# Optimization experiments

Measured on AMD Instinct MI355X. Metric: run time of the kernel, lower is better.

## Reference

```python
import jax, jax.numpy as jnp
import numpy as np

B, C, H, W = 4, 256, 64, 64
CQK = C // 8  # qk_downscale = 8


def setup_inputs() -> dict:
    key = jax.random.key(0)
    ks = jax.random.split(key, 4)
    scale = 0.02
    x = jax.random.normal(ks[0], (B, C, H, W), dtype=jnp.float32)
    Wq = jax.random.normal(ks[1], (CQK, C), dtype=jnp.float32) * scale
    bq = jnp.zeros((CQK,), dtype=jnp.float32)
    Wk = jax.random.normal(ks[2], (CQK, C), dtype=jnp.float32) * scale
    bk = jnp.zeros((CQK,), dtype=jnp.float32)
    Wv = jax.random.normal(ks[3], (C, C), dtype=jnp.float32) * scale
    bv = jnp.zeros((C,), dtype=jnp.float32)
    gamma = jnp.ones((1,), dtype=jnp.float32)
    return {"x": x, "Wq": Wq, "bq": bq, "Wk": Wk, "bk": bk,
            "Wv": Wv, "bv": bv, "gamma": gamma}


def reference(x, Wq, bq, Wk, bk, Wv, bv, gamma):
    b, c, h, w = x.shape
    n = h * w
    xf = x.reshape(b, c, n)                                   # [B,C,N]
    # 1x1 Conv1d == per-position linear projection
    q = jnp.einsum('oc,bcn->bon', Wq, xf) + bq[:, None]        # [B,C/8,N]
    k = jnp.einsum('oc,bcn->bon', Wk, xf) + bk[:, None]        # [B,C/8,N]
    v = jnp.einsum('oc,bcn->bon', Wv, xf) + bv[:, None]        # [B,C,N]
    # scores[b,i,j] = sum_c q[b,c,i] * k[b,c,j]  (bmm(q^T, k))
    scores = jnp.einsum('bci,bcj->bij', q, k)                  # [B,N,N]
    # softmax over dim=1 (the i / contracted axis) — SAGAN style, no 1/sqrt(d)
    attn = jax.nn.softmax(scores, axis=1)                      # [B,N,N]
    out = gamma * jnp.einsum('bcn,bnm->bcm', v, attn) + xf     # [B,C,N]
    return out.reshape(b, c, h, w)
```

## Files before the change

### kernel.cpp

```cpp
#include <hip/hip_runtime.h>
#include <stdint.h>

typedef __attribute__((ext_vector_type(8))) short short8;
typedef __attribute__((ext_vector_type(4))) float f32x4;
typedef __attribute__((ext_vector_type(4))) unsigned int u32x4;

#define MFMA16(a, b, c) __builtin_amdgcn_mfma_f32_16x16x32_bf16((a), (b), (c), 0, 0, 0)

#define GLOAD_LDS16(gsrc, ldst)                                                        \
    __builtin_amdgcn_global_load_lds(                                                  \
        (const __attribute__((address_space(1))) unsigned int*)(gsrc),                 \
        (__attribute__((address_space(3))) unsigned int*)(ldst), 16, 0, 0)

#define LOG2E 1.4426950408889634f

static __device__ __forceinline__ unsigned short f2bf(float f) {
    union { float f; unsigned int u; } v; v.f = f;
    unsigned int u = v.u;
    unsigned int r = 0x7fffu + ((u >> 16) & 1u);
    return (unsigned short)((u + r) >> 16);
}

static __device__ __forceinline__ float bf2f(unsigned short s) {
    union { unsigned int u; float f; } v; v.u = ((unsigned int)s) << 16;
    return v.f;
}

static __device__ __forceinline__ unsigned int cvt_pk_bf16(float lo, float hi) {
    unsigned int r;
    asm("v_cvt_pk_bf16_f32 %0, %1, %2" : "=v"(r) : "v"(lo), "v"(hi));
    return r;
}

static __device__ __forceinline__ float fexp2(float x) {
#if __has_builtin(__builtin_amdgcn_exp2f)
    return __builtin_amdgcn_exp2f(x);
#else
    return exp2f(x);
#endif
}

__global__ __launch_bounds__(256) void k_prepw(const float* __restrict__ Wq,
                                               const float* __restrict__ Wk,
                                               const float* __restrict__ Wv,
                                               unsigned short* __restrict__ Wb) {
    const int i = (blockIdx.x * 256 + threadIdx.x) * 4;
    const float* src; int off;
    if (i < 8192)       { src = Wq; off = i; }
    else if (i < 16384) { src = Wk; off = i - 8192; }
    else                { src = Wv; off = i - 16384; }
    const float4 v = *(const float4*)(src + off);
    ushort4 o;
    o.x = f2bf(v.x); o.y = f2bf(v.y); o.z = f2bf(v.z); o.w = f2bf(v.w);
    *(ushort4*)(Wb + i) = o;
}

__global__ __launch_bounds__(256) void k_qkv(const float* __restrict__ x,
                                             const unsigned short* __restrict__ Wb,
                                             const float* __restrict__ bq,
                                             const float* __restrict__ bk,
                                             const float* __restrict__ bv,
                                             unsigned short* __restrict__ qT,
                                             unsigned short* __restrict__ kT,
                                             unsigned short* __restrict__ vp) {
    const int b = blockIdx.y;
    const int nt = blockIdx.x;
    const int h = blockIdx.z;
    const int lane = threadIdx.x & 63;
    const int wv = threadIdx.x >> 6;
    const int l15 = lane & 15, g = lane >> 4;
    const int n0 = nt * 64;
    const int nw = n0 + wv * 16;

    const float* xb = x + (size_t)b * 1048576;
    const float* xs = xb + (size_t)(g * 8) * 4096 + nw + l15;

    const unsigned short* Wqb = Wb;
    const unsigned short* Wkb = Wb + 8192;
    const unsigned short* Wvb = Wb + 16384 + h * 32768;

    f32x4 aqk[4] = {};
    f32x4 av[8] = {};

#pragma unroll 2
    for (int k0 = 0; k0 < 256; k0 += 32) {
        const float* xp = xs + (size_t)k0 * 4096;
        float xv[8];
#pragma unroll
        for (int j = 0; j < 8; ++j) xv[j] = xp[(size_t)j * 4096];
        const u32x4 ux = {cvt_pk_bf16(xv[0], xv[1]), cvt_pk_bf16(xv[2], xv[3]),
                          cvt_pk_bf16(xv[4], xv[5]), cvt_pk_bf16(xv[6], xv[7])};
        const short8 xa = __builtin_bit_cast(short8, ux);

        if (h == 0) {
#pragma unroll
            for (int ot = 0; ot < 4; ++ot) {
                const unsigned short* wr = (ot < 2) ? (Wqb + (size_t)(ot * 16 + l15) * 256)
                                                    : (Wkb + (size_t)((ot - 2) * 16 + l15) * 256);
                const short8 wb8 = *(const short8*)(wr + k0 + g * 8);
                aqk[ot] = MFMA16(xa, wb8, aqk[ot]);
            }
        }
#pragma unroll
        for (int ct = 0; ct < 8; ++ct) {
            const short8 wv8 = *(const short8*)(Wvb + (size_t)(ct * 16 + l15) * 256 + k0 + g * 8);
            av[ct] = MFMA16(wv8, xa, av[ct]);
        }
    }

    if (h == 0) {
#pragma unroll
        for (int ot = 0; ot < 4; ++ot) {
            const int o = (ot & 1) * 16 + l15;
            const float bias = (ot < 2) ? bq[o] : bk[o];
            const float sc = (ot < 2) ? LOG2E : 1.0f;
            unsigned short* dst = (ot < 2) ? qT : kT;
#pragma unroll
            for (int r = 0; r < 4; ++r) {
                const int n = nw + g * 4 + r;
                dst[((size_t)b * 4096 + n) * 32 + o] = f2bf((aqk[ot][r] + bias) * sc);
            }
        }
    }
    const int jp = ((wv >> 1) * 4 + (l15 >> 2)) * 8 + (wv & 1) * 4 + (l15 & 3);
#pragma unroll
    for (int ct = 0; ct < 8; ++ct)
#pragma unroll
        for (int r = 0; r < 4; ++r) {
            const int c = h * 128 + ct * 16 + g * 4 + r;
            vp[((size_t)b * 256 + c) * 4096 + n0 + jp] = f2bf(av[ct][r] + bv[c]);
        }
}

__global__ __launch_bounds__(256, 2) void k_attn(const unsigned short* __restrict__ qT,
                                                 const unsigned short* __restrict__ kT,
                                                 const unsigned short* __restrict__ vp,
                                                 unsigned short* __restrict__ Opart,
                                                 float* __restrict__ mll,
                                                 int ilen) {
    __shared__ __align__(16) unsigned short vlds[2 * 16384];

    const int b = blockIdx.y;
    const int mt = blockIdx.x;
    const int sp = blockIdx.z;
    const int tid = threadIdx.x;
    const int lane = tid & 63;
    const int wv = tid >> 6;
    const int l15 = lane & 15, g = lane >> 4;
    const int m_base = mt * 128 + wv * 32;
    const int i_start = sp * ilen;
    const int T = ilen >> 6;

    const unsigned short* qTb = qT + (size_t)b * 131072;
    const unsigned short* vpb = vp + (size_t)b * 1048576;

    const short8 qkB0 = *(const short8*)(kT + ((size_t)b * 4096 + m_base + l15) * 32 + g * 8);
    const short8 qkB1 = *(const short8*)(kT + ((size_t)b * 4096 + m_base + 16 + l15) * 32 + g * 8);

    const int jd = (lane & 7) ^ ((lane >> 3) & 7);
    const unsigned short* vsrc = vpb + (size_t)(64 * wv + (lane >> 3)) * 4096 + i_start + jd * 8;
    const int ldst0 = wv * 4096;

#define STAGE(bufsel, ioff)                                                             \
    do {                                                                                \
        _Pragma("unroll")                                                               \
        for (int s_ = 0; s_ < 8; ++s_)                                                  \
            GLOAD_LDS16(vsrc + (size_t)s_ * 32768 + (ioff),                             \
                        vlds + (bufsel) * 16384 + ldst0 + s_ * 512);                    \
    } while (0)

    const int rdA = l15 * 64 + ((g ^ (l15 & 7)) << 3);
    const int rdB = l15 * 64 + (((4 + g) ^ (l15 & 7)) << 3);

    const unsigned short* qp = qTb + (size_t)(i_start + l15) * 32 + g * 8;

    f32x4 oacc[16][2] = {};
    float l_acc0 = 0.0f, l_acc1 = 0.0f;
    const f32x4 zf = {0.f, 0.f, 0.f, 0.f};

    STAGE(0, 0);
    __syncthreads();

    for (int t = 0; t < T; ++t) {
        const int cur = t & 1;
        if (t + 1 < T) STAGE(cur ^ 1, (t + 1) * 64);

        const short8 a0 = *(const short8*)(qp);
        const short8 a1 = *(const short8*)(qp + 512);
        const short8 a2 = *(const short8*)(qp + 1024);
        const short8 a3 = *(const short8*)(qp + 1536);
        qp += 2048;
        f32x4 P[4][2];
        P[0][0] = MFMA16(a0, qkB0, zf); P[0][1] = MFMA16(a0, qkB1, zf);
        P[1][0] = MFMA16(a1, qkB0, zf); P[1][1] = MFMA16(a1, qkB1, zf);
        P[2][0] = MFMA16(a2, qkB0, zf); P[2][1] = MFMA16(a2, qkB1, zf);
        P[3][0] = MFMA16(a3, qkB0, zf); P[3][1] = MFMA16(a3, qkB1, zf);

        float s00 = 0.f, s01 = 0.f, s10 = 0.f, s11 = 0.f;
#pragma unroll
        for (int it = 0; it < 4; ++it)
#pragma unroll
            for (int r = 0; r < 4; ++r) {
                P[it][0][r] = fexp2(P[it][0][r]);
                P[it][1][r] = fexp2(P[it][1][r]);
                if (it < 2) { s00 += P[it][0][r]; s01 += P[it][1][r]; }
                else        { s10 += P[it][0][r]; s11 += P[it][1][r]; }
            }
        l_acc0 += s00 + s10;
        l_acc1 += s01 + s11;

        const u32x4 u00 = {cvt_pk_bf16(P[0][0][0], P[0][0][1]), cvt_pk_bf16(P[0][0][2], P[0][0][3]),
                           cvt_pk_bf16(P[1][0][0], P[1][0][1]), cvt_pk_bf16(P[1][0][2], P[1][0][3])};
        const u32x4 u01 = {cvt_pk_bf16(P[0][1][0], P[0][1][1]), cvt_pk_bf16(P[0][1][2], P[0][1][3]),
                           cvt_pk_bf16(P[1][1][0], P[1][1][1]), cvt_pk_bf16(P[1][1][2], P[1][1][3])};
        const u32x4 u10 = {cvt_pk_bf16(P[2][0][0], P[2][0][1]), cvt_pk_bf16(P[2][0][2], P[2][0][3]),
                           cvt_pk_bf16(P[3][0][0], P[3][0][1]), cvt_pk_bf16(P[3][0][2], P[3][0][3])};
        const u32x4 u11 = {cvt_pk_bf16(P[2][1][0], P[2][1][1]), cvt_pk_bf16(P[2][1][2], P[2][1][3]),
                           cvt_pk_bf16(P[3][1][0], P[3][1][1]), cvt_pk_bf16(P[3][1][2], P[3][1][3])};
        const short8 pb00 = __builtin_bit_cast(short8, u00);
        const short8 pb01 = __builtin_bit_cast(short8, u01);
        const short8 pb10 = __builtin_bit_cast(short8, u10);
        const short8 pb11 = __builtin_bit_cast(short8, u11);

        const unsigned short* vbase = vlds + cur * 16384;
        const unsigned short* pA = vbase + rdA;
        const unsigned short* pB = vbase + rdB;
        __builtin_amdgcn_s_setprio(1);
#pragma unroll
        for (int ct = 0; ct < 16; ++ct) {
            const short8 va0 = *(const short8*)(pA + ct * 1024);
            const short8 va1 = *(const short8*)(pB + ct * 1024);
            oacc[ct][0] = MFMA16(va0, pb00, oacc[ct][0]);
            oacc[ct][1] = MFMA16(va0, pb01, oacc[ct][1]);
            oacc[ct][0] = MFMA16(va1, pb10, oacc[ct][0]);
            oacc[ct][1] = MFMA16(va1, pb11, oacc[ct][1]);
        }
        __builtin_amdgcn_s_setprio(0);

        if (t + 1 < T) __syncthreads();
    }
#undef STAGE

    unsigned short* Ob = Opart + (size_t)(sp * 4 + b) * 1048576;
#pragma unroll
    for (int ct = 0; ct < 16; ++ct)
#pragma unroll
        for (int r = 0; r < 4; ++r) {
            const int c = ct * 16 + g * 4 + r;
            Ob[(size_t)c * 4096 + m_base + l15]      = f2bf(oacc[ct][0][r]);
            Ob[(size_t)c * 4096 + m_base + 16 + l15] = f2bf(oacc[ct][1][r]);
        }
    float l0 = l_acc0, l1 = l_acc1;
    l0 += __shfl_xor(l0, 16); l0 += __shfl_xor(l0, 32);
    l1 += __shfl_xor(l1, 16); l1 += __shfl_xor(l1, 32);
    if (lane < 16) {
        const size_t mi = (size_t)(sp * 4 + b) * 4096 + m_base + l15;
        mll[mi]      = l0;
        mll[mi + 16] = l1;
    }
}

__global__ __launch_bounds__(256) void k_combine(const unsigned short* __restrict__ Opart,
                                                 const float* __restrict__ mll,
                                                 const float* __restrict__ x,
                                                 const float* __restrict__ gamma,
                                                 float* __restrict__ out, int S) {
    const size_t e0 = ((size_t)blockIdx.x * 256 + threadIdx.x) * 8;
    const int m0 = (int)(e0 & 4095);
    const int b = (int)(e0 >> 20);

    float L[8] = {}, O[8] = {};
    for (int s = 0; s < S; ++s) {
        const size_t base = (size_t)(s * 4 + b) * 4096 + m0;
        const float4 la = *(const float4*)(mll + base);
        const float4 lc = *(const float4*)(mll + base + 4);
        const short8 op = *(const short8*)(Opart + (size_t)s * 4194304 + e0);
        L[0] += la.x; O[0] += bf2f((unsigned short)op[0]);
        L[1] += la.y; O[1] += bf2f((unsigned short)op[1]);
        L[2] += la.z; O[2] += bf2f((unsigned short)op[2]);
        L[3] += la.w; O[3] += bf2f((unsigned short)op[3]);
        L[4] += lc.x; O[4] += bf2f((unsigned short)op[4]);
        L[5] += lc.y; O[5] += bf2f((unsigned short)op[5]);
        L[6] += lc.z; O[6] += bf2f((unsigned short)op[6]);
        L[7] += lc.w; O[7] += bf2f((unsigned short)op[7]);
    }

    const float g0 = gamma[0];
    const float4 x0 = *(const float4*)(x + e0);
    const float4 x1 = *(const float4*)(x + e0 + 4);
    float4 o0, o1;
    o0.x = g0 * O[0] / L[0] + x0.x; o0.y = g0 * O[1] / L[1] + x0.y;
    o0.z = g0 * O[2] / L[2] + x0.z; o0.w = g0 * O[3] / L[3] + x0.w;
    o1.x = g0 * O[4] / L[4] + x1.x; o1.y = g0 * O[5] / L[5] + x1.y;
    o1.z = g0 * O[6] / L[6] + x1.z; o1.w = g0 * O[7] / L[7] + x1.w;
    *(float4*)(out + e0) = o0;
    *(float4*)(out + e0 + 4) = o1;
}

extern "C" void kernel_launch(void* const* d_in, const int* in_sizes, int n_in,
                              void* d_out, int out_size, void* d_ws, size_t ws_size,
                              hipStream_t stream) {
    (void)in_sizes; (void)n_in; (void)out_size;
    const float* x     = (const float*)d_in[0];
    const float* Wq    = (const float*)d_in[1];
    const float* bq    = (const float*)d_in[2];
    const float* Wk    = (const float*)d_in[3];
    const float* bk    = (const float*)d_in[4];
    const float* Wv    = (const float*)d_in[5];
    const float* bv    = (const float*)d_in[6];
    const float* gamma = (const float*)d_in[7];
    float* out = (float*)d_out;

    unsigned short* qT = (unsigned short*)d_ws;
    unsigned short* kT = qT + (size_t)4 * 4096 * 32;
    unsigned short* vp = kT + (size_t)4 * 4096 * 32;
    unsigned short* Wb = vp + (size_t)4 * 256 * 4096;
    unsigned short* Opart = Wb + 81920;

    const size_t base_el = 2 * (size_t)4 * 4096 * 32 + (size_t)4 * 256 * 4096 + 81920;
    auto need = [&](int s) {
        return (base_el + (size_t)s * 4194304) * 2 + (size_t)s * 16384 * 4;
    };
    const int S = (need(4) <= ws_size) ? 4 : (need(2) <= ws_size) ? 2 : 1;
    float* mll = (float*)(Opart + (size_t)S * 4194304);

    k_prepw<<<dim3(80), 256, 0, stream>>>(Wq, Wk, Wv, Wb);
    k_qkv<<<dim3(64, 4, 2), 256, 0, stream>>>(x, Wb, bq, bk, bv, qT, kT, vp);
    k_attn<<<dim3(32, 4, S), 256, 0, stream>>>(qT, kT, vp, Opart, mll, 4096 / S);
    k_combine<<<dim3(2048), 256, 0, stream>>>(Opart, mll, x, gamma, out, S);
}
```

Before: 84.35 us.

## Switch attention kernel to 32x32x16 MFMA tiles with matching V permutation

Rewrites the attention inner loop to use 32x32x16 bf16 MFMA instead of 16x16x32, so each wave computes one 32-column score tile and accumulates output in 8 f32x16 accumulators. The V projection output permutation and the LDS read offsets are changed to match the new operand layout, and the row-sum reduction shrinks to a single shuffle. The aim is fewer MFMA issues and fewer LDS reads per unit of work, and higher operand reuse. The cost is a different register pressure profile and a dependent chain of four MFMAs per accumulator.

New measurement: 86.41 us. 2.4% more time.

```diff
diff --git a/kernel.cpp b/kernel.cpp
--- a/kernel.cpp
+++ b/kernel.cpp
@@ -3,9 +3,11 @@
 
 typedef __attribute__((ext_vector_type(8))) short short8;
 typedef __attribute__((ext_vector_type(4))) float f32x4;
+typedef __attribute__((ext_vector_type(16))) float f32x16;
 typedef __attribute__((ext_vector_type(4))) unsigned int u32x4;
 
 #define MFMA16(a, b, c) __builtin_amdgcn_mfma_f32_16x16x32_bf16((a), (b), (c), 0, 0, 0)
+#define MFMA32(a, b, c) __builtin_amdgcn_mfma_f32_32x32x16_bf16((a), (b), (c), 0, 0, 0)
 
 #define GLOAD_LDS16(gsrc, ldst)                                                        \
     __builtin_amdgcn_global_load_lds(                                                  \
@@ -122,7 +124,7 @@
             }
         }
     }
-    const int jp = ((wv >> 1) * 4 + (l15 >> 2)) * 8 + (wv & 1) * 4 + (l15 & 3);
+    const int jp = (2 * wv + ((l15 >> 2) & 1)) * 8 + (l15 & 3) + ((l15 >> 3) << 2);
 #pragma unroll
     for (int ct = 0; ct < 8; ++ct)
 #pragma unroll
@@ -146,7 +148,7 @@
     const int tid = threadIdx.x;
     const int lane = tid & 63;
     const int wv = tid >> 6;
-    const int l15 = lane & 15, g = lane >> 4;
+    const int l31 = lane & 31, h = lane >> 5;
     const int m_base = mt * 128 + wv * 32;
     const int i_start = sp * ilen;
     const int T = ilen >> 6;
@@ -154,8 +156,9 @@
     const unsigned short* qTb = qT + (size_t)b * 131072;
     const unsigned short* vpb = vp + (size_t)b * 1048576;
 
-    const short8 qkB0 = *(const short8*)(kT + ((size_t)b * 4096 + m_base + l15) * 32 + g * 8);
-    const short8 qkB1 = *(const short8*)(kT + ((size_t)b * 4096 + m_base + 16 + l15) * 32 + g * 8);
+    const unsigned short* krow = kT + ((size_t)b * 4096 + m_base + l31) * 32 + h * 8;
+    const short8 qkB0 = *(const short8*)(krow);
+    const short8 qkB1 = *(const short8*)(krow + 16);
 
     const int jd = (lane & 7) ^ ((lane >> 3) & 7);
     const unsigned short* vsrc = vpb + (size_t)(64 * wv + (lane >> 3)) * 4096 + i_start + jd * 8;
@@ -169,14 +172,18 @@
                         vlds + (bufsel) * 16384 + ldst0 + s_ * 512);                    \
     } while (0)
 
-    const int rdA = l15 * 64 + ((g ^ (l15 & 7)) << 3);
-    const int rdB = l15 * 64 + (((4 + g) ^ (l15 & 7)) << 3);
-
-    const unsigned short* qp = qTb + (size_t)(i_start + l15) * 32 + g * 8;
-
-    f32x4 oacc[16][2] = {};
-    float l_acc0 = 0.0f, l_acc1 = 0.0f;
-    const f32x4 zf = {0.f, 0.f, 0.f, 0.f};
+    const int rd0 = l31 * 64 + (((2 * 0 + h) ^ (l31 & 7)) << 3);
+    const int rd1 = l31 * 64 + (((2 * 1 + h) ^ (l31 & 7)) << 3);
+    const int rd2 = l31 * 64 + (((2 * 2 + h) ^ (l31 & 7)) << 3);
+    const int rd3 = l31 * 64 + (((2 * 3 + h) ^ (l31 & 7)) << 3);
+
+    const unsigned short* qp = qTb + (size_t)(i_start + l31) * 32 + h * 8;
+
+    f32x16 oacc[8] = {};
+    float l_acc = 0.0f;
+    f32x16 zf16;
+#pragma unroll
+    for (int r = 0; r < 16; ++r) zf16[r] = 0.0f;
 
     STAGE(0, 0);
     __syncthreads();
@@ -185,55 +192,50 @@
         const int cur = t & 1;
         if (t + 1 < T) STAGE(cur ^ 1, (t + 1) * 64);
 
-        const short8 a0 = *(const short8*)(qp);
-        const short8 a1 = *(const short8*)(qp + 512);
-        const short8 a2 = *(const short8*)(qp + 1024);
-        const short8 a3 = *(const short8*)(qp + 1536);
+        const short8 qa00 = *(const short8*)(qp);
+        const short8 qa01 = *(const short8*)(qp + 16);
+        const short8 qa10 = *(const short8*)(qp + 1024);
+        const short8 qa11 = *(const short8*)(qp + 1040);
         qp += 2048;
-        f32x4 P[4][2];
-        P[0][0] = MFMA16(a0, qkB0, zf); P[0][1] = MFMA16(a0, qkB1, zf);
-        P[1][0] = MFMA16(a1, qkB0, zf); P[1][1] = MFMA16(a1, qkB1, zf);
-        P[2][0] = MFMA16(a2, qkB0, zf); P[2][1] = MFMA16(a2, qkB1, zf);
-        P[3][0] = MFMA16(a3, qkB0, zf); P[3][1] = MFMA16(a3, qkB1, zf);
-
-        float s00 = 0.f, s01 = 0.f, s10 = 0.f, s11 = 0.f;
-#pragma unroll
-        for (int it = 0; it < 4; ++it)
-#pragma unroll
-            for (int r = 0; r < 4; ++r) {
-                P[it][0][r] = fexp2(P[it][0][r]);
-                P[it][1][r] = fexp2(P[it][1][r]);
-                if (it < 2) { s00 += P[it][0][r]; s01 += P[it][1][r]; }
-                else        { s10 += P[it][0][r]; s11 += P[it][1][r]; }
-            }
-        l_acc0 += s00 + s10;
-        l_acc1 += s01 + s11;
-
-        const u32x4 u00 = {cvt_pk_bf16(P[0][0][0], P[0][0][1]), cvt_pk_bf16(P[0][0][2], P[0][0][3]),
-                           cvt_pk_bf16(P[1][0][0], P[1][0][1]), cvt_pk_bf16(P[1][0][2], P[1][0][3])};
-        const u32x4 u01 = {cvt_pk_bf16(P[0][1][0], P[0][1][1]), cvt_pk_bf16(P[0][1][2], P[0][1][3]),
-                           cvt_pk_bf16(P[1][1][0], P[1][1][1]), cvt_pk_bf16(P[1][1][2], P[1][1][3])};
-        const u32x4 u10 = {cvt_pk_bf16(P[2][0][0], P[2][0][1]), cvt_pk_bf16(P[2][0][2], P[2][0][3]),
-                           cvt_pk_bf16(P[3][0][0], P[3][0][1]), cvt_pk_bf16(P[3][0][2], P[3][0][3])};
-        const u32x4 u11 = {cvt_pk_bf16(P[2][1][0], P[2][1][1]), cvt_pk_bf16(P[2][1][2], P[2][1][3]),
-                           cvt_pk_bf16(P[3][1][0], P[3][1][1]), cvt_pk_bf16(P[3][1][2], P[3][1][3])};
-        const short8 pb00 = __builtin_bit_cast(short8, u00);
-        const short8 pb01 = __builtin_bit_cast(short8, u01);
-        const short8 pb10 = __builtin_bit_cast(short8, u10);
-        const short8 pb11 = __builtin_bit_cast(short8, u11);
-
-        const unsigned short* vbase = vlds + cur * 16384;
-        const unsigned short* pA = vbase + rdA;
-        const unsigned short* pB = vbase + rdB;
+        f32x16 P0 = MFMA32(qa00, qkB0, zf16);
+        P0 = MFMA32(qa01, qkB1, P0);
+        f32x16 P1 = MFMA32(qa10, qkB0, zf16);
+        P1 = MFMA32(qa11, qkB1, P1);
+
+        float s = 0.f;
+#pragma unroll
+        for (int r = 0; r < 16; ++r) {
+            P0[r] = fexp2(P0[r]); s += P0[r];
+            P1[r] = fexp2(P1[r]); s += P1[r];
+        }
+        l_acc += s;
+
+        const u32x4 u0 = {cvt_pk_bf16(P0[0], P0[1]), cvt_pk_bf16(P0[2], P0[3]),
+                          cvt_pk_bf16(P0[4], P0[5]), cvt_pk_bf16(P0[6], P0[7])};
+        const u32x4 u1 = {cvt_pk_bf16(P0[8], P0[9]), cvt_pk_bf16(P0[10], P0[11]),
+                          cvt_pk_bf16(P0[12], P0[13]), cvt_pk_bf16(P0[14], P0[15])};
+        const u32x4 u2 = {cvt_pk_bf16(P1[0], P1[1]), cvt_pk_bf16(P1[2], P1[3]),
+                          cvt_pk_bf16(P1[4], P1[5]), cvt_pk_bf16(P1[6], P1[7])};
+        const u32x4 u3 = {cvt_pk_bf16(P1[8], P1[9]), cvt_pk_bf16(P1[10], P1[11]),
+                          cvt_pk_bf16(P1[12], P1[13]), cvt_pk_bf16(P1[14], P1[15])};
+        const short8 pb0 = __builtin_bit_cast(short8, u0);
+        const short8 pb1 = __builtin_bit_cast(short8, u1);
+        const short8 pb2 = __builtin_bit_cast(short8, u2);
+        const short8 pb3 = __builtin_bit_cast(short8, u3);
+
+        const unsigned short* vb = vlds + cur * 16384;
         __builtin_amdgcn_s_setprio(1);
 #pragma unroll
-        for (int ct = 0; ct < 16; ++ct) {
-            const short8 va0 = *(const short8*)(pA + ct * 1024);
-            const short8 va1 = *(const short8*)(pB + ct * 1024);
-            oacc[ct][0] = MFMA16(va0, pb00, oacc[ct][0]);
-            oacc[ct][1] = MFMA16(va0, pb01, oacc[ct][1]);
-            oacc[ct][0] = MFMA16(va1, pb10, oacc[ct][0]);
-            oacc[ct][1] = MFMA16(va1, pb11, oacc[ct][1]);
+        for (int cb = 0; cb < 8; ++cb) {
+            const unsigned short* vr = vb + cb * 2048;
+            const short8 va0 = *(const short8*)(vr + rd0);
+            const short8 va1 = *(const short8*)(vr + rd1);
+            const short8 va2 = *(const short8*)(vr + rd2);
+            const short8 va3 = *(const short8*)(vr + rd3);
+            oacc[cb] = MFMA32(va0, pb0, oacc[cb]);
+            oacc[cb] = MFMA32(va1, pb1, oacc[cb]);
+            oacc[cb] = MFMA32(va2, pb2, oacc[cb]);
+            oacc[cb] = MFMA32(va3, pb3, oacc[cb]);
         }
         __builtin_amdgcn_s_setprio(0);
 
@@ -243,20 +245,15 @@
 
     unsigned short* Ob = Opart + (size_t)(sp * 4 + b) * 1048576;
 #pragma unroll
-    for (int ct = 0; ct < 16; ++ct)
-#pragma unroll
-        for (int r = 0; r < 4; ++r) {
-            const int c = ct * 16 + g * 4 + r;
-            Ob[(size_t)c * 4096 + m_base + l15]      = f2bf(oacc[ct][0][r]);
-            Ob[(size_t)c * 4096 + m_base + 16 + l15] = f2bf(oacc[ct][1][r]);
-        }
-    float l0 = l_acc0, l1 = l_acc1;
-    l0 += __shfl_xor(l0, 16); l0 += __shfl_xor(l0, 32);
-    l1 += __shfl_xor(l1, 16); l1 += __shfl_xor(l1, 32);
-    if (lane < 16) {
-        const size_t mi = (size_t)(sp * 4 + b) * 4096 + m_base + l15;
-        mll[mi]      = l0;
-        mll[mi + 16] = l1;
+    for (int cb = 0; cb < 8; ++cb)
+#pragma unroll
+        for (int r = 0; r < 16; ++r) {
+            const int c = cb * 32 + (r & 3) + 8 * (r >> 2) + 4 * h;
+            Ob[(size_t)c * 4096 + m_base + l31] = f2bf(oacc[cb][r]);
+        }
+    float l0 = l_acc + __shfl_xor(l_acc, 32);
+    if (lane < 32) {
+        mll[(size_t)(sp * 4 + b) * 4096 + m_base + l31] = l0;
     }
 }
 
```

## Split attention K-tile across wave pairs with LDS reduction of accumulators

Applied to the files above, without the earlier changes.

k_attn now launches 512 threads per block, and each pair of waves splits the 64-wide i-chunk of each tile in half. Each wave computes half the scores and exp values and does half the PV MFMAs, and each wave also stages half as much V into LDS. At the end the two halves' fp32 accumulators and row sums are added through LDS in two passes before one wave writes the result. The aim is more waves in flight per block to hide latency, at the cost of extra barriers, an LDS reduction epilogue, and only one block per CU under the launch bounds.

Result: slower. 105.8 us (+25.5%).

```diff
diff --git a/kernel.cpp b/kernel.cpp
--- a/kernel.cpp
+++ b/kernel.cpp
@@ -132,7 +132,7 @@
         }
 }
 
-__global__ __launch_bounds__(256, 2) void k_attn(const unsigned short* __restrict__ qT,
+__global__ __launch_bounds__(512, 1) void k_attn(const unsigned short* __restrict__ qT,
                                                  const unsigned short* __restrict__ kT,
                                                  const unsigned short* __restrict__ vp,
                                                  unsigned short* __restrict__ Opart,
@@ -146,8 +146,9 @@
     const int tid = threadIdx.x;
     const int lane = tid & 63;
     const int wv = tid >> 6;
+    const int mg = wv >> 1, sl = wv & 1;
     const int l15 = lane & 15, g = lane >> 4;
-    const int m_base = mt * 128 + wv * 32;
+    const int m_base = mt * 128 + mg * 32;
     const int i_start = sp * ilen;
     const int T = ilen >> 6;
 
@@ -158,21 +159,20 @@
     const short8 qkB1 = *(const short8*)(kT + ((size_t)b * 4096 + m_base + 16 + l15) * 32 + g * 8);
 
     const int jd = (lane & 7) ^ ((lane >> 3) & 7);
-    const unsigned short* vsrc = vpb + (size_t)(64 * wv + (lane >> 3)) * 4096 + i_start + jd * 8;
-    const int ldst0 = wv * 4096;
+    const unsigned short* vsrc = vpb + (size_t)(32 * wv + (lane >> 3)) * 4096 + i_start + jd * 8;
+    const int ldst0 = wv * 2048;
 
 #define STAGE(bufsel, ioff)                                                             \
     do {                                                                                \
         _Pragma("unroll")                                                               \
-        for (int s_ = 0; s_ < 8; ++s_)                                                  \
+        for (int s_ = 0; s_ < 4; ++s_)                                                  \
             GLOAD_LDS16(vsrc + (size_t)s_ * 32768 + (ioff),                             \
                         vlds + (bufsel) * 16384 + ldst0 + s_ * 512);                    \
     } while (0)
 
-    const int rdA = l15 * 64 + ((g ^ (l15 & 7)) << 3);
-    const int rdB = l15 * 64 + (((4 + g) ^ (l15 & 7)) << 3);
-
-    const unsigned short* qp = qTb + (size_t)(i_start + l15) * 32 + g * 8;
+    const int rdA = l15 * 64 + (((4 * sl + g) ^ (l15 & 7)) << 3);
+
+    const unsigned short* qp = qTb + (size_t)(i_start + sl * 32 + l15) * 32 + g * 8;
 
     f32x4 oacc[16][2] = {};
     float l_acc0 = 0.0f, l_acc1 = 0.0f;
@@ -187,53 +187,36 @@
 
         const short8 a0 = *(const short8*)(qp);
         const short8 a1 = *(const short8*)(qp + 512);
-        const short8 a2 = *(const short8*)(qp + 1024);
-        const short8 a3 = *(const short8*)(qp + 1536);
         qp += 2048;
-        f32x4 P[4][2];
+        f32x4 P[2][2];
         P[0][0] = MFMA16(a0, qkB0, zf); P[0][1] = MFMA16(a0, qkB1, zf);
         P[1][0] = MFMA16(a1, qkB0, zf); P[1][1] = MFMA16(a1, qkB1, zf);
-        P[2][0] = MFMA16(a2, qkB0, zf); P[2][1] = MFMA16(a2, qkB1, zf);
-        P[3][0] = MFMA16(a3, qkB0, zf); P[3][1] = MFMA16(a3, qkB1, zf);
-
-        float s00 = 0.f, s01 = 0.f, s10 = 0.f, s11 = 0.f;
-#pragma unroll
-        for (int it = 0; it < 4; ++it)
+
+        float s0 = 0.f, s1 = 0.f;
+#pragma unroll
+        for (int it = 0; it < 2; ++it)
 #pragma unroll
             for (int r = 0; r < 4; ++r) {
-                P[it][0][r] = fexp2(P[it][0][r]);
-                P[it][1][r] = fexp2(P[it][1][r]);
-                if (it < 2) { s00 += P[it][0][r]; s01 += P[it][1][r]; }
-                else        { s10 += P[it][0][r]; s11 += P[it][1][r]; }
-            }
-        l_acc0 += s00 + s10;
-        l_acc1 += s01 + s11;
-
-        const u32x4 u00 = {cvt_pk_bf16(P[0][0][0], P[0][0][1]), cvt_pk_bf16(P[0][0][2], P[0][0][3]),
-                           cvt_pk_bf16(P[1][0][0], P[1][0][1]), cvt_pk_bf16(P[1][0][2], P[1][0][3])};
-        const u32x4 u01 = {cvt_pk_bf16(P[0][1][0], P[0][1][1]), cvt_pk_bf16(P[0][1][2], P[0][1][3]),
-                           cvt_pk_bf16(P[1][1][0], P[1][1][1]), cvt_pk_bf16(P[1][1][2], P[1][1][3])};
-        const u32x4 u10 = {cvt_pk_bf16(P[2][0][0], P[2][0][1]), cvt_pk_bf16(P[2][0][2], P[2][0][3]),
-                           cvt_pk_bf16(P[3][0][0], P[3][0][1]), cvt_pk_bf16(P[3][0][2], P[3][0][3])};
-        const u32x4 u11 = {cvt_pk_bf16(P[2][1][0], P[2][1][1]), cvt_pk_bf16(P[2][1][2], P[2][1][3]),
-                           cvt_pk_bf16(P[3][1][0], P[3][1][1]), cvt_pk_bf16(P[3][1][2], P[3][1][3])};
-        const short8 pb00 = __builtin_bit_cast(short8, u00);
-        const short8 pb01 = __builtin_bit_cast(short8, u01);
-        const short8 pb10 = __builtin_bit_cast(short8, u10);
-        const short8 pb11 = __builtin_bit_cast(short8, u11);
-
-        const unsigned short* vbase = vlds + cur * 16384;
-        const unsigned short* pA = vbase + rdA;
-        const unsigned short* pB = vbase + rdB;
+                P[it][0][r] = fexp2(P[it][0][r]); s0 += P[it][0][r];
+                P[it][1][r] = fexp2(P[it][1][r]); s1 += P[it][1][r];
+            }
+        l_acc0 += s0;
+        l_acc1 += s1;
+
+        const u32x4 u0 = {cvt_pk_bf16(P[0][0][0], P[0][0][1]), cvt_pk_bf16(P[0][0][2], P[0][0][3]),
+                          cvt_pk_bf16(P[1][0][0], P[1][0][1]), cvt_pk_bf16(P[1][0][2], P[1][0][3])};
+        const u32x4 u1 = {cvt_pk_bf16(P[0][1][0], P[0][1][1]), cvt_pk_bf16(P[0][1][2], P[0][1][3]),
+                          cvt_pk_bf16(P[1][1][0], P[1][1][1]), cvt_pk_bf16(P[1][1][2], P[1][1][3])};
+        const short8 pb0 = __builtin_bit_cast(short8, u0);
+        const short8 pb1 = __builtin_bit_cast(short8, u1);
+
+        const unsigned short* pA = vlds + cur * 16384 + rdA;
         __builtin_amdgcn_s_setprio(1);
 #pragma unroll
         for (int ct = 0; ct < 16; ++ct) {
-            const short8 va0 = *(const short8*)(pA + ct * 1024);
-            const short8 va1 = *(const short8*)(pB + ct * 1024);
-            oacc[ct][0] = MFMA16(va0, pb00, oacc[ct][0]);
-            oacc[ct][1] = MFMA16(va0, pb01, oacc[ct][1]);
-            oacc[ct][0] = MFMA16(va1, pb10, oacc[ct][0]);
-            oacc[ct][1] = MFMA16(va1, pb11, oacc[ct][1]);
+            const short8 va = *(const short8*)(pA + ct * 1024);
+            oacc[ct][0] = MFMA16(va, pb0, oacc[ct][0]);
+            oacc[ct][1] = MFMA16(va, pb1, oacc[ct][1]);
         }
         __builtin_amdgcn_s_setprio(0);
 
@@ -241,22 +224,71 @@
     }
 #undef STAGE
 
-    unsigned short* Ob = Opart + (size_t)(sp * 4 + b) * 1048576;
-#pragma unroll
-    for (int ct = 0; ct < 16; ++ct)
-#pragma unroll
-        for (int r = 0; r < 4; ++r) {
-            const int c = ct * 16 + g * 4 + r;
-            Ob[(size_t)c * 4096 + m_base + l15]      = f2bf(oacc[ct][0][r]);
-            Ob[(size_t)c * 4096 + m_base + 16 + l15] = f2bf(oacc[ct][1][r]);
-        }
-    float l0 = l_acc0, l1 = l_acc1;
-    l0 += __shfl_xor(l0, 16); l0 += __shfl_xor(l0, 32);
-    l1 += __shfl_xor(l1, 16); l1 += __shfl_xor(l1, 32);
-    if (lane < 16) {
-        const size_t mi = (size_t)(sp * 4 + b) * 4096 + m_base + l15;
-        mll[mi]      = l0;
-        mll[mi + 16] = l1;
+    float* red = (float*)vlds;
+    __syncthreads();
+    if (sl == 1) {
+#pragma unroll
+        for (int ct = 0; ct < 8; ++ct)
+#pragma unroll
+            for (int ms = 0; ms < 2; ++ms)
+                *(f32x4*)(red + mg * 4096 + (ct * 2 + ms) * 256 + lane * 4) = oacc[ct][ms];
+    }
+    __syncthreads();
+    if (sl == 0) {
+#pragma unroll
+        for (int ct = 0; ct < 8; ++ct)
+#pragma unroll
+            for (int ms = 0; ms < 2; ++ms) {
+                const f32x4 v = *(const f32x4*)(red + mg * 4096 + (ct * 2 + ms) * 256 + lane * 4);
+                oacc[ct][ms] += v;
+            }
+    }
+    __syncthreads();
+    if (sl == 1) {
+#pragma unroll
+        for (int ct = 0; ct < 8; ++ct)
+#pragma unroll
+            for (int ms = 0; ms < 2; ++ms)
+                *(f32x4*)(red + mg * 4096 + (ct * 2 + ms) * 256 + lane * 4) = oacc[ct + 8][ms];
+    }
+    __syncthreads();
+    if (sl == 0) {
+#pragma unroll
+        for (int ct = 0; ct < 8; ++ct)
+#pragma unroll
+            for (int ms = 0; ms < 2; ++ms) {
+                const f32x4 v = *(const f32x4*)(red + mg * 4096 + (ct * 2 + ms) * 256 + lane * 4);
+                oacc[ct + 8][ms] += v;
+            }
+    }
+    __syncthreads();
+    if (sl == 1) {
+        red[mg * 128 + lane * 2]     = l_acc0;
+        red[mg * 128 + lane * 2 + 1] = l_acc1;
+    }
+    __syncthreads();
+
+    if (sl == 0) {
+        l_acc0 += red[mg * 128 + lane * 2];
+        l_acc1 += red[mg * 128 + lane * 2 + 1];
+
+        unsigned short* Ob = Opart + (size_t)(sp * 4 + b) * 1048576;
+#pragma unroll
+        for (int ct = 0; ct < 16; ++ct)
+#pragma unroll
+            for (int r = 0; r < 4; ++r) {
+                const int c = ct * 16 + g * 4 + r;
+                Ob[(size_t)c * 4096 + m_base + l15]      = f2bf(oacc[ct][0][r]);
+                Ob[(size_t)c * 4096 + m_base + 16 + l15] = f2bf(oacc[ct][1][r]);
+            }
+        float l0 = l_acc0, l1 = l_acc1;
+        l0 += __shfl_xor(l0, 16); l0 += __shfl_xor(l0, 32);
+        l1 += __shfl_xor(l1, 16); l1 += __shfl_xor(l1, 32);
+        if (lane < 16) {
+            const size_t mi = (size_t)(sp * 4 + b) * 4096 + m_base + l15;
+            mll[mi]      = l0;
+            mll[mi + 16] = l1;
+        }
     }
 }
 
@@ -326,6 +358,6 @@
 
     k_prepw<<<dim3(80), 256, 0, stream>>>(Wq, Wk, Wv, Wb);
     k_qkv<<<dim3(64, 4, 2), 256, 0, stream>>>(x, Wb, bq, bk, bv, qT, kT, vp);
-    k_attn<<<dim3(32, 4, S), 256, 0, stream>>>(qT, kT, vp, Opart, mll, 4096 / S);
+    k_attn<<<dim3(32, 4, S), 512, 0, stream>>>(qT, kT, vp, Opart, mll, 4096 / S);
     k_combine<<<dim3(2048), 256, 0, stream>>>(Opart, mll, x, gamma, out, S);
 }
```
